# Optimization experiments

Hardware: AMD Instinct MI355X
Metric: run time of the kernel (lower is better)

Reference implementation:

```python
import jax, jax.numpy as jnp
import numpy as np

B, S, H, NH, DH, I, C, P = 4, 1024, 1280, 20, 64, 5120, 13, 8
LN_EPS = 1e-5


def setup_inputs() -> dict:
    key = jax.random.key(0)
    ks = jax.random.split(key, 20)
    n = lambda k, shp, s=0.02: (jax.random.normal(k, shp, jnp.float32) * s)
    return {
        "hidden_states": jax.random.normal(ks[0], (B, S, H), jnp.float32),
        "attention_mask": jnp.ones((B, S), jnp.float32),
        "Wq": n(ks[1], (H, H)), "bq": jnp.zeros((H,), jnp.float32),
        "Wk": n(ks[2], (H, H)), "bk": jnp.zeros((H,), jnp.float32),
        "Wv": n(ks[3], (H, H)), "bv": jnp.zeros((H,), jnp.float32),
        "W_ct1": n(ks[4], (P, C), 0.3), "b_ct1": jnp.zeros((P,), jnp.float32),
        "W_ct2": n(ks[5], (P, C), 0.3), "b_ct2": jnp.zeros((P,), jnp.float32),
        "M": n(ks[6], (C, C), 0.5),
        "bias_scale": jnp.full((1,), 0.5, jnp.float32),
        "W_ptm": n(ks[7], (P, H)), "b_ptm": jnp.zeros((P,), jnp.float32),
        "ln_g": jnp.ones((H,), jnp.float32), "ln_b": jnp.zeros((H,), jnp.float32),
        "Wf1": n(ks[8], (I, H)), "bf1": jnp.zeros((I,), jnp.float32),
        "Wf2": n(ks[9], (H, I)), "bf2": jnp.zeros((H,), jnp.float32),
    }


def reference(hidden_states, attention_mask, Wq, bq, Wk, bk, Wv, bv,
              W_ct1, b_ct1, W_ct2, b_ct2, M, bias_scale, W_ptm, b_ptm,
              ln_g, ln_b, Wf1, bf1, Wf2, bf2):
    h = hidden_states
    # crosstalk bilinear projection: (P,C) @ (C,P) -> (P,P)
    out1 = (M.T @ W_ct1.T + b_ct1).T          # (P, C)
    out2 = M @ W_ct2.T + b_ct2                # (C, P)
    R = out1 @ out2                           # (P, P)
    # ptm_predictor (Linear H->P) + softmax
    ptm = jax.nn.softmax(h @ W_ptm.T + b_ptm, axis=-1)            # (B,S,P)
    Bb = jnp.tanh(jnp.einsum('blc,cd,bmd->blm', ptm, R, ptm)) * bias_scale  # (B,S,S)
    # manual multi-head attention
    q = (h @ Wq.T + bq).reshape(B, S, NH, DH).transpose(0, 2, 1, 3)
    k = (h @ Wk.T + bk).reshape(B, S, NH, DH).transpose(0, 2, 1, 3)
    v = (h @ Wv.T + bv).reshape(B, S, NH, DH).transpose(0, 2, 1, 3)
    scores = jnp.einsum('bhld,bhmd->bhlm', q, k) / np.float32(np.sqrt(DH))
    scores = scores + Bb[:, None]
    scores = scores + (1.0 - attention_mask)[:, None, None, :] * jnp.finfo(h.dtype).min
    probs = jax.nn.softmax(scores, axis=-1)
    ctx = jnp.einsum('bhlm,bhmd->bhld', probs, v)
    ctx = ctx.transpose(0, 2, 1, 3).reshape(B, S, H)
    # residual + LayerNorm
    x = h + ctx
    mu = jnp.mean(x, -1, keepdims=True)
    var = jnp.var(x, -1, keepdims=True)
    x = (x - mu) * jax.lax.rsqrt(var + LN_EPS) * ln_g + ln_b
    # FFN with exact GELU, residual
    ff = jax.nn.gelu(x @ Wf1.T + bf1, approximate=False) @ Wf2.T + bf2
    return x + ff
```

## Files before the change

### kernel.cpp

```cpp
#include <hip/hip_runtime.h>
#include <math.h>

typedef _Float16 f16;
typedef _Float16 f16x2 __attribute__((ext_vector_type(2)));
typedef _Float16 f16x8 __attribute__((ext_vector_type(8)));
typedef _Float16 f16x4 __attribute__((ext_vector_type(4)));
typedef float f32x4 __attribute__((ext_vector_type(4)));

#define B_ 4
#define S_ 1024
#define H_ 1280
#define NH_ 20
#define DH_ 64
#define I_ 5120
#define C_ 13
#define P_ 8
#define QS_ 3840
#define LOG2E 1.44269504088896f

__device__ __forceinline__ void store_val(float* p, float v) { *p = v; }
__device__ __forceinline__ void store_val(f16* p, float v) { *p = (f16)v; }

__device__ __forceinline__ float fast_gelu(float x) {
    float ax = 0.70710678118654752f * fabsf(x);
    float t = __builtin_amdgcn_rcpf(1.0f + 0.3275911f * ax);
    float p = t * (0.254829592f + t * (-0.284496736f + t * (1.421413741f
              + t * (-1.453152027f + t * 1.061405429f))));
    float e = __builtin_exp2f(-(LOG2E) * ax * ax);
    float er = 1.0f - p * e;
    float cdf = 0.5f + 0.5f * (x >= 0.0f ? er : -er);
    return x * cdf;
}

__device__ __forceinline__ float fast_tanh(float x) {
    x = fminf(fmaxf(x, -20.0f), 20.0f);
    float e = __builtin_exp2f(x * (2.0f * LOG2E));
    return (e - 1.0f) * __builtin_amdgcn_rcpf(e + 1.0f);
}

__global__ __launch_bounds__(256) void prep_kernel(const float* __restrict__ hin,
                                                   const float* __restrict__ Wptm,
                                                   const float* __restrict__ bptm,
                                                   const float* __restrict__ Mg,
                                                   const float* __restrict__ W1,
                                                   const float* __restrict__ b1,
                                                   const float* __restrict__ W2,
                                                   const float* __restrict__ b2,
                                                   float* __restrict__ ptm,
                                                   float* __restrict__ tg,
                                                   f16* __restrict__ hin16,
                                                   const float* __restrict__ Wq,
                                                   const float* __restrict__ Wk,
                                                   const float* __restrict__ Wv,
                                                   const float* __restrict__ Wf1,
                                                   const float* __restrict__ Wf2,
                                                   f16* __restrict__ Wq16,
                                                   f16* __restrict__ Wk16,
                                                   f16* __restrict__ Wv16,
                                                   f16* __restrict__ Wf116,
                                                   f16* __restrict__ Wf216) {
    const int bid = blockIdx.x;
    int t = threadIdx.x;
    if (bid >= 1024) {
        const int cb = bid - 1024;
        const float* src; f16* dst; int base;
        if (cb < 4800) {
            const int s = cb / 1600;
            src = (s == 0) ? Wq : (s == 1) ? Wk : Wv;
            dst = (s == 0) ? Wq16 : (s == 1) ? Wk16 : Wv16;
            base = (cb - s * 1600) * 256;
        } else if (cb < 11200) {
            src = Wf1; dst = Wf116; base = (cb - 4800) * 256;
        } else {
            src = Wf2; dst = Wf216; base = (cb - 11200) * 256;
        }
        const int i = base + t;
        f32x4 v = ((const f32x4*)src)[i];
        f16x4 o;
#pragma unroll
        for (int e = 0; e < 4; e++) o[e] = (f16)v[e];
        ((f16x4*)dst)[i] = o;
        return;
    }

    __shared__ float o1[P_][C_];
    __shared__ float o2[C_][P_];
    __shared__ float R[P_ * P_];
    if (t < P_ * C_) {
        int p = t / C_, c = t % C_;
        float s = b1[p];
        for (int k = 0; k < C_; k++) s += Mg[k * C_ + c] * W1[p * C_ + k];
        o1[p][c] = s;
        int c2 = t / P_, p2 = t % P_;
        float s2 = b2[p2];
        for (int k = 0; k < C_; k++) s2 += Mg[c2 * C_ + k] * W2[p2 * C_ + k];
        o2[c2][p2] = s2;
    }
    __syncthreads();
    if (t < P_ * P_) {
        int p = t >> 3, q = t & 7;
        float s = 0.f;
        for (int c = 0; c < C_; c++) s += o1[p][c] * o2[c][q];
        R[t] = s;
    }
    __syncthreads();

    int wv = t >> 6, lane = t & 63;
    int row = bid * 4 + wv;
    const float* hrow = hin + (size_t)row * H_;
    f16* hrow16 = hin16 + (size_t)row * H_;
    float acc[P_] = {};
    for (int i = 0; i < H_ / 64; i++) {
        int k = lane + 64 * i;
        float hv = hrow[k];
        hrow16[k] = (f16)hv;
#pragma unroll
        for (int p = 0; p < P_; p++) acc[p] += hv * Wptm[p * H_ + k];
    }
#pragma unroll
    for (int p = 0; p < P_; p++) {
#pragma unroll
        for (int o = 32; o >= 1; o >>= 1) acc[p] += __shfl_xor(acc[p], o);
        acc[p] += bptm[p];
    }
    float mx = acc[0];
#pragma unroll
    for (int p = 1; p < P_; p++) mx = fmaxf(mx, acc[p]);
    float sum = 0.f;
#pragma unroll
    for (int p = 0; p < P_; p++) { acc[p] = expf(acc[p] - mx); sum += acc[p]; }
    float rinv = 1.f / sum;
#pragma unroll
    for (int p = 0; p < P_; p++) acc[p] *= rinv;
    float tv[P_];
#pragma unroll
    for (int d = 0; d < P_; d++) {
        float s = 0.f;
#pragma unroll
        for (int c = 0; c < P_; c++) s += acc[c] * R[c * P_ + d];
        tv[d] = s;
    }
    if (lane == 0) {
#pragma unroll
        for (int p = 0; p < P_; p++) {
            ptm[(size_t)row * P_ + p] = acc[p];
            tg[(size_t)row * P_ + p]  = tv[p];
        }
    }
}

__global__ __launch_bounds__(256) void bias_kernel(const float* __restrict__ tg,
                                                   const float* __restrict__ ptm,
                                                   const float* __restrict__ mask,
                                                   const float* __restrict__ bscale_p,
                                                   f16* __restrict__ bb) {
    const int bl = blockIdx.x;
    const int b = bl >> 10;
    const int t = threadIdx.x;
    __shared__ float tl[P_];
    if (t < P_) tl[t] = tg[(size_t)bl * P_ + t];
    __syncthreads();
    const float bscale = bscale_p[0];
    float t0 = tl[0], t1 = tl[1], t2 = tl[2], t3 = tl[3];
    float t4 = tl[4], t5 = tl[5], t6 = tl[6], t7 = tl[7];
#pragma unroll
    for (int i = 0; i < 4; i++) {
        int m = t + 256 * i;
        const float* pm = ptm + ((size_t)b * S_ + m) * P_;
        float4 p0 = *(const float4*)pm;
        float4 p1 = *(const float4*)(pm + 4);
        float d = t0 * p0.x + t1 * p0.y + t2 * p0.z + t3 * p0.w
                + t4 * p1.x + t5 * p1.y + t6 * p1.z + t7 * p1.w;
        float v = (fast_tanh(d) * bscale + (1.0f - mask[(size_t)b * S_ + m]) * (-30000.0f)) * LOG2E;
        bb[(size_t)bl * S_ + m] = (f16)v;
    }
}

template <int MODE, typename YT>
__device__ __forceinline__ void gemm_body(const f16* __restrict__ X,
                                          const f16* __restrict__ W,
                                          const float* __restrict__ bias,
                                          YT* __restrict__ Y,
                                          int Ndim, int Kdim, int kbeg, int kend,
                                          int m0, int n0, f16* sA, f16* sB) {
    const int t = threadIdx.x;
    const int lane = t & 63, w = t >> 6;
    const int wr = w >> 1, wc = w & 1;
    const int lr = lane & 15, kq = lane >> 4;

    f32x4 acc[4][4] = {};

    int s_row[4], s_gc[4];
#pragma unroll
    for (int inst = 0; inst < 4; inst++) {
        int ci = t + 256 * inst;
        s_row[inst] = ci >> 3;
        s_gc[inst] = (ci & 7) ^ (s_row[inst] & 7);
    }

    for (int k0 = kbeg; k0 < kend; k0 += 64) {
        __syncthreads();
#pragma unroll
        for (int inst = 0; inst < 4; inst++) {
            int ci = t + 256 * inst;
            __builtin_amdgcn_global_load_lds(
                (const unsigned*)(X + (size_t)(m0 + s_row[inst]) * Kdim + k0 + s_gc[inst] * 8),
                (unsigned*)(sA + ci * 8), 16, 0, 0);
        }
#pragma unroll
        for (int inst = 0; inst < 4; inst++) {
            int ci = t + 256 * inst;
            __builtin_amdgcn_global_load_lds(
                (const unsigned*)(W + (size_t)(n0 + s_row[inst]) * Kdim + k0 + s_gc[inst] * 8),
                (unsigned*)(sB + ci * 8), 16, 0, 0);
        }
        __syncthreads();
#pragma unroll
        for (int ks = 0; ks < 2; ks++) {
            f16x8 af[4], bf[4];
#pragma unroll
            for (int i = 0; i < 4; i++) {
                int row = wr * 64 + i * 16 + lr;
                int cl = (ks * 4 + kq) ^ (row & 7);
                af[i] = *(const f16x8*)(sA + row * 64 + cl * 8);
            }
#pragma unroll
            for (int j = 0; j < 4; j++) {
                int row = wc * 64 + j * 16 + lr;
                int cl = (ks * 4 + kq) ^ (row & 7);
                bf[j] = *(const f16x8*)(sB + row * 64 + cl * 8);
            }
#pragma unroll
            for (int i = 0; i < 4; i++)
#pragma unroll
                for (int j = 0; j < 4; j++)
                    acc[i][j] = __builtin_amdgcn_mfma_f32_16x16x32_f16(af[i], bf[j], acc[i][j], 0, 0, 0);
        }
    }
#pragma unroll
    for (int j = 0; j < 4; j++) {
        int col = n0 + wc * 64 + j * 16 + lr;
        float bcol = bias[col];
#pragma unroll
        for (int i = 0; i < 4; i++) {
#pragma unroll
            for (int rr = 0; rr < 4; rr++) {
                int row = m0 + wr * 64 + i * 16 + kq * 4 + rr;
                float v = acc[i][j][rr] + bcol;
                if (MODE == 1) v = fast_gelu(v);
                store_val(&Y[(size_t)row * Ndim + col], v);
            }
        }
    }
}

template <int MODE, typename YT>
__global__ __launch_bounds__(256, 2) void gemm128(const f16* __restrict__ X,
                                                  const f16* __restrict__ W,
                                                  const float* __restrict__ bias,
                                                  YT* __restrict__ Y,
                                                  int Ndim, int Kdim) {
    __shared__ f16 sA[128 * 64];
    __shared__ f16 sB[128 * 64];
    gemm_body<MODE, YT>(X, W, bias, Y, Ndim, Kdim, 0, Kdim,
                        blockIdx.x * 128, blockIdx.y * 128, sA, sB);
}

template <int MODE, typename YT>
__device__ __forceinline__ void g256_body(const f16* __restrict__ X,
                                          const f16* __restrict__ W,
                                          const float* __restrict__ bias,
                                          YT* __restrict__ Y,
                                          int Ndim, int Kdim, int kbeg, int kend,
                                          int m0, int n0, f16* sA, f16* sB) {
    const int NT = (kend - kbeg) >> 6;
    const int t = threadIdx.x;
    const int lane = t & 63, w = t >> 6;
    const int wr = w >> 2, wc = w & 3;
    const int lr = lane & 15, kq = lane >> 4;

    const int rh0 = t >> 3;
    const int gc0 = (t & 7) ^ (rh0 & 7);
    const f16* Asrc = X + (size_t)(m0 + rh0) * Kdim + kbeg + gc0 * 8;
    const f16* Bsrc = W + (size_t)(n0 + rh0) * Kdim + kbeg + gc0 * 8;

    f32x4 acc[8][4] = {};

#define STG_A(kt_) do { f16* d_ = sA + ((kt_) & 1) * 16384 + t * 8;            \
        const f16* s_ = Asrc + (size_t)(kt_) * 64;                             \
        __builtin_amdgcn_global_load_lds((const unsigned*)s_, (unsigned*)d_, 16, 0, 0); \
        __builtin_amdgcn_global_load_lds((const unsigned*)(s_ + (size_t)64 * Kdim),  (unsigned*)(d_ + 4096), 16, 0, 0);  \
        __builtin_amdgcn_global_load_lds((const unsigned*)(s_ + (size_t)128 * Kdim), (unsigned*)(d_ + 8192), 16, 0, 0);  \
        __builtin_amdgcn_global_load_lds((const unsigned*)(s_ + (size_t)192 * Kdim), (unsigned*)(d_ + 12288), 16, 0, 0); \
    } while (0)
#define STG_B(kt_) do { f16* d_ = sB + ((kt_) & 1) * 16384 + t * 8;            \
        const f16* s_ = Bsrc + (size_t)(kt_) * 64;                             \
        __builtin_amdgcn_global_load_lds((const unsigned*)s_, (unsigned*)d_, 16, 0, 0); \
        __builtin_amdgcn_global_load_lds((const unsigned*)(s_ + (size_t)64 * Kdim),  (unsigned*)(d_ + 4096), 16, 0, 0);  \
        __builtin_amdgcn_global_load_lds((const unsigned*)(s_ + (size_t)128 * Kdim), (unsigned*)(d_ + 8192), 16, 0, 0);  \
        __builtin_amdgcn_global_load_lds((const unsigned*)(s_ + (size_t)192 * Kdim), (unsigned*)(d_ + 12288), 16, 0, 0); \
    } while (0)

    STG_A(0); STG_B(0);
    if (NT > 1) {
        STG_A(1); STG_B(1);
        asm volatile("s_waitcnt vmcnt(8)");
    } else {
        asm volatile("s_waitcnt vmcnt(0)");
    }
    __builtin_amdgcn_s_barrier();

    for (int kt = 0; kt < NT; ++kt) {
        const int p = kt & 1;
        const f16* cA = sA + p * 16384;
        const f16* cB = sB + p * 16384;
        f16x8 a[4][2], b0[2][2], b1[2][2];

#pragma unroll
        for (int i = 0; i < 4; ++i) {
            const int r = wr * 128 + (i + 4) * 16 + lr;
#pragma unroll
            for (int ks = 0; ks < 2; ++ks)
                a[i][ks] = *(const f16x8*)(cA + r * 64 + (((ks * 4 + kq) ^ (r & 7)) * 8));
        }
#pragma unroll
        for (int j = 0; j < 2; ++j) {
            const int rb = wc * 64 + j * 16 + lr;
#pragma unroll
            for (int ks = 0; ks < 2; ++ks)
                b0[j][ks] = *(const f16x8*)(cB + rb * 64 + (((ks * 4 + kq) ^ (rb & 7)) * 8));
        }
        __builtin_amdgcn_s_barrier();
        __builtin_amdgcn_s_setprio(1);
#pragma unroll
        for (int ks = 0; ks < 2; ++ks)
#pragma unroll
            for (int i = 0; i < 4; ++i)
#pragma unroll
                for (int j = 0; j < 2; ++j)
                    acc[i + 4][j] = __builtin_amdgcn_mfma_f32_16x16x32_f16(
                        a[i][ks], b0[j][ks], acc[i + 4][j], 0, 0, 0);
        __builtin_amdgcn_s_setprio(0);
        __builtin_amdgcn_s_barrier();

#pragma unroll
        for (int j = 0; j < 2; ++j) {
            const int rb = wc * 64 + (j + 2) * 16 + lr;
#pragma unroll
            for (int ks = 0; ks < 2; ++ks)
                b1[j][ks] = *(const f16x8*)(cB + rb * 64 + (((ks * 4 + kq) ^ (rb & 7)) * 8));
        }
        __builtin_amdgcn_s_barrier();
        __builtin_amdgcn_s_setprio(1);
#pragma unroll
        for (int ks = 0; ks < 2; ++ks)
#pragma unroll
            for (int i = 0; i < 4; ++i)
#pragma unroll
                for (int j = 0; j < 2; ++j)
                    acc[i + 4][j + 2] = __builtin_amdgcn_mfma_f32_16x16x32_f16(
                        a[i][ks], b1[j][ks], acc[i + 4][j + 2], 0, 0, 0);
        __builtin_amdgcn_s_setprio(0);
        __builtin_amdgcn_s_barrier();

#pragma unroll
        for (int i = 0; i < 4; ++i) {
            const int r = wr * 128 + i * 16 + lr;
#pragma unroll
            for (int ks = 0; ks < 2; ++ks)
                a[i][ks] = *(const f16x8*)(cA + r * 64 + (((ks * 4 + kq) ^ (r & 7)) * 8));
        }
        if (kt + 2 < NT) STG_B(kt + 2);
        __builtin_amdgcn_s_barrier();
        __builtin_amdgcn_s_setprio(1);
#pragma unroll
        for (int ks = 0; ks < 2; ++ks)
#pragma unroll
            for (int i = 0; i < 4; ++i)
#pragma unroll
                for (int j = 0; j < 2; ++j)
                    acc[i][j] = __builtin_amdgcn_mfma_f32_16x16x32_f16(
                        a[i][ks], b0[j][ks], acc[i][j], 0, 0, 0);
        __builtin_amdgcn_s_setprio(0);
        __builtin_amdgcn_s_barrier();

        if (kt + 2 < NT) STG_A(kt + 2);
        __builtin_amdgcn_s_setprio(1);
#pragma unroll
        for (int ks = 0; ks < 2; ++ks)
#pragma unroll
            for (int i = 0; i < 4; ++i)
#pragma unroll
                for (int j = 0; j < 2; ++j)
                    acc[i][j + 2] = __builtin_amdgcn_mfma_f32_16x16x32_f16(
                        a[i][ks], b1[j][ks], acc[i][j + 2], 0, 0, 0);
        __builtin_amdgcn_s_setprio(0);
        if (kt + 2 < NT) asm volatile("s_waitcnt vmcnt(8)");
        else             asm volatile("s_waitcnt vmcnt(0)");
        __builtin_amdgcn_s_barrier();
    }
#undef STG_A
#undef STG_B

#pragma unroll
    for (int j = 0; j < 4; ++j) {
        const int col = n0 + wc * 64 + j * 16 + lr;
        const float bcol = (MODE == 3) ? 0.f : bias[col];
#pragma unroll
        for (int i = 0; i < 8; ++i) {
#pragma unroll
            for (int rr = 0; rr < 4; ++rr) {
                const int row = m0 + wr * 128 + i * 16 + kq * 4 + rr;
                float v = acc[i][j][rr] + bcol;
                store_val(&Y[(size_t)row * Ndim + col], v);
            }
        }
    }
}

__global__ __launch_bounds__(512, 2) void gemm256_sk(const f16* __restrict__ X,
                                                     const f16* __restrict__ W,
                                                     float* __restrict__ p0,
                                                     float* __restrict__ p1,
                                                     float* __restrict__ p2,
                                                     int Ndim, int Kdim) {
    __shared__ f16 sA[2 * 16384];
    __shared__ f16 sB[2 * 16384];
    const int z = blockIdx.z;
    float* __restrict__ Y = (z == 0) ? p0 : (z == 1) ? p1 : p2;
    const int kbeg = z * 1728;
    const int kend = (z == 2) ? Kdim : kbeg + 1728;
    g256_body<3, float>(X, W, nullptr, Y, Ndim, Kdim, kbeg, kend,
                        blockIdx.x * 256, blockIdx.y * 256, sA, sB);
}

__global__ __launch_bounds__(512, 2) void gemm256_qkv(const f16* __restrict__ X,
                                                      const f16* __restrict__ Wqkv,
                                                      const float* __restrict__ bq,
                                                      const float* __restrict__ bk,
                                                      const float* __restrict__ bv,
                                                      f16* __restrict__ Y) {
    __shared__ f16 sA[2 * 16384];
    __shared__ f16 sB[2 * 16384];
    const int nt = blockIdx.y;
    const int g = nt / 5;
    const float* bsel = (g == 0) ? bq : (g == 1) ? bk : bv;
    g256_body<0, f16>(X, Wqkv, bsel - (size_t)g * 1280, Y, QS_, H_, 0, H_,
                      blockIdx.x * 256, nt * 256, sA, sB);
}

__global__ __launch_bounds__(256) void reduce3_kernel(const float* __restrict__ p0,
                                                      const float* __restrict__ p1,
                                                      const float* __restrict__ p2,
                                                      const float* __restrict__ bias,
                                                      const f16* __restrict__ res,
                                                      float* __restrict__ out) {
    int i = blockIdx.x * 256 + threadIdx.x;
    int col = (i * 4) % H_;
    f32x4 a = ((const f32x4*)p0)[i];
    f32x4 b = ((const f32x4*)p1)[i];
    f32x4 c = ((const f32x4*)p2)[i];
    f32x4 bc = *(const f32x4*)(bias + col);
    f16x4 r = ((const f16x4*)res)[i];
    f32x4 o;
#pragma unroll
    for (int e = 0; e < 4; e++) o[e] = a[e] + b[e] + c[e] + bc[e] + (float)r[e];
    ((f32x4*)out)[i] = o;
}

__global__ __launch_bounds__(256) void attn_kernel(const f16* __restrict__ qkv,
                                                   const f16* __restrict__ bb,
                                                   const float* __restrict__ hin,
                                                   float* __restrict__ xpre) {
    __shared__ f16 sK[64 * 72];
    __shared__ f16 sVT[64 * 72];
    __shared__ f16 sP[64 * 72];

    const int t = threadIdx.x;
    const int w = t >> 6, lane = t & 63;
    const int lr = lane & 15, kq = lane >> 4;
    const int gid = blockIdx.x + 16 * (blockIdx.y + 20 * blockIdx.z);
    const int wk = (gid & 7) * 160 + (gid >> 3);
    const int l0 = (wk & 15) * 64;
    const int hb = wk >> 4;
    const int h = hb % 20, b = hb / 20;
    const size_t base  = (size_t)b * S_ * H_ + (size_t)h * DH_;
    const size_t baseq = (size_t)b * S_ * QS_ + (size_t)h * DH_;
    const size_t kbase = baseq + 1280;
    const size_t vbase = baseq + 2560;

    const int kr0 = t >> 3, kc8 = (t & 7) * 8;
    const int vr2 = (t >> 3) * 2, vc8 = (t & 7) * 8;
    const int vmsw = vr2 ^ vc8;
    const int br = t >> 2, bc16 = (t & 3) * 16;
    const f16* bbrow0 = bb + ((size_t)b * S_ + l0 + br) * S_;

    f16x8 kA0 = *(const f16x8*)&qkv[kbase + (size_t)kr0 * QS_ + kc8];
    f16x8 kA1 = *(const f16x8*)&qkv[kbase + (size_t)(kr0 + 32) * QS_ + kc8];
    f16x8 vA0 = *(const f16x8*)&qkv[vbase + (size_t)vr2 * QS_ + vc8];
    f16x8 vA1 = *(const f16x8*)&qkv[vbase + (size_t)(vr2 + 1) * QS_ + vc8];
    f16x8 bA0 = *(const f16x8*)(bbrow0 + bc16);
    f16x8 bA1 = *(const f16x8*)(bbrow0 + bc16 + 8);

    f16x8 afq[2];
#pragma unroll
    for (int ks = 0; ks < 2; ks++) {
        f16x8 qv = *(const f16x8*)&qkv[baseq + (size_t)(l0 + w * 16 + lr) * QS_ + ks * 32 + kq * 8];
#pragma unroll
        for (int e = 0; e < 8; e++) qv[e] = (f16)((float)qv[e] * (0.125f * LOG2E));
        afq[ks] = qv;
    }

    f32x4 acc_o[4] = {};
    float lstate[4] = {};

    for (int mt = 0; mt < 16; mt++) {
        __syncthreads();
        *(f16x8*)&sK[kr0 * 72 + kc8] = kA0;
        *(f16x8*)&sK[(kr0 + 32) * 72 + kc8] = kA1;
#pragma unroll
        for (int e = 0; e < 8; e++) {
            f16x2 pk = {vA0[e], vA1[e]};
            *(f16x2*)&sVT[(vc8 + e) * 72 + vmsw] = pk;
        }
        *(f16x8*)&sP[br * 72 + bc16] = bA0;
        *(f16x8*)&sP[br * 72 + bc16 + 8] = bA1;
        const int m1 = ((mt + 1) & 15) * 64;
        f16x8 kB0 = *(const f16x8*)&qkv[kbase + (size_t)(m1 + kr0) * QS_ + kc8];
        f16x8 kB1 = *(const f16x8*)&qkv[kbase + (size_t)(m1 + kr0 + 32) * QS_ + kc8];
        f16x8 vB0 = *(const f16x8*)&qkv[vbase + (size_t)(m1 + vr2) * QS_ + vc8];
        f16x8 vB1 = *(const f16x8*)&qkv[vbase + (size_t)(m1 + vr2 + 1) * QS_ + vc8];
        f16x8 bB0 = *(const f16x8*)(bbrow0 + m1 + bc16);
        f16x8 bB1 = *(const f16x8*)(bbrow0 + m1 + bc16 + 8);
        __syncthreads();

        f32x4 sacc[4] = {};
        __builtin_amdgcn_s_setprio(1);
#pragma unroll
        for (int ks = 0; ks < 2; ks++)
#pragma unroll
            for (int j = 0; j < 4; j++) {
                f16x8 bk = *(const f16x8*)&sK[(j * 16 + lr) * 72 + ks * 32 + kq * 8];
                sacc[j] = __builtin_amdgcn_mfma_f32_16x16x32_f16(afq[ks], bk, sacc[j], 0, 0, 0);
            }
        __builtin_amdgcn_s_setprio(0);

#pragma unroll
        for (int j = 0; j < 4; j++)
#pragma unroll
            for (int rr = 0; rr < 4; rr++) {
                const int sp_addr = (w * 16 + kq * 4 + rr) * 72 + j * 16 + lr;
                float p = __builtin_exp2f(sacc[j][rr] + (float)sP[sp_addr]);
                lstate[rr] += p;
                sP[sp_addr] = (f16)p;
            }

        f16x8 ap[2];
        ap[0] = *(const f16x8*)&sP[(w * 16 + lr) * 72 + kq * 8];
        ap[1] = *(const f16x8*)&sP[(w * 16 + lr) * 72 + 32 + kq * 8];
        __builtin_amdgcn_s_setprio(1);
#pragma unroll
        for (int ks = 0; ks < 2; ks++)
#pragma unroll
            for (int j2 = 0; j2 < 4; j2++) {
                int d = j2 * 16 + lr;
                int s_ = (d >> 3) & 7;
                f16x8 bv = *(const f16x8*)&sVT[d * 72 + 8 * (((ks << 2) + kq) ^ s_)];
                acc_o[j2] = __builtin_amdgcn_mfma_f32_16x16x32_f16(ap[ks], bv, acc_o[j2], 0, 0, 0);
            }
        __builtin_amdgcn_s_setprio(0);
        kA0 = kB0; kA1 = kB1; vA0 = vB0; vA1 = vB1; bA0 = bB0; bA1 = bB1;
    }

#pragma unroll
    for (int rr = 0; rr < 4; rr++) {
#pragma unroll
        for (int off = 8; off >= 1; off >>= 1) lstate[rr] += __shfl_xor(lstate[rr], off);
    }

#pragma unroll
    for (int rr = 0; rr < 4; rr++) {
        float linv = 1.0f / lstate[rr];
        int tok = l0 + w * 16 + kq * 4 + rr;
        size_t obase = base + (size_t)tok * H_;
#pragma unroll
        for (int j2 = 0; j2 < 4; j2++) {
            int d = j2 * 16 + lr;
            xpre[obase + d] = hin[obase + d] + acc_o[j2][rr] * linv;
        }
    }
}

__global__ __launch_bounds__(256) void ln_kernel(const float* __restrict__ xpre,
                                                 const float* __restrict__ g,
                                                 const float* __restrict__ bb,
                                                 f16* __restrict__ xln) {
    int row = blockIdx.x, t = threadIdx.x;
    const float* xr = xpre + (size_t)row * H_;
    float xv[5], s1 = 0.f, s2 = 0.f;
#pragma unroll
    for (int i = 0; i < 5; i++) {
        float v = xr[t + 256 * i];
        xv[i] = v; s1 += v; s2 += v * v;
    }
#pragma unroll
    for (int o = 32; o >= 1; o >>= 1) { s1 += __shfl_xor(s1, o); s2 += __shfl_xor(s2, o); }
    __shared__ float r1[4], r2[4];
    int wv = t >> 6, lane = t & 63;
    if (lane == 0) { r1[wv] = s1; r2[wv] = s2; }
    __syncthreads();
    float m1 = (r1[0] + r1[1] + r1[2] + r1[3]) * (1.0f / H_);
    float m2 = (r2[0] + r2[1] + r2[2] + r2[3]) * (1.0f / H_);
    float rstd = rsqrtf(m2 - m1 * m1 + 1e-5f);
#pragma unroll
    for (int i = 0; i < 5; i++) {
        int c = t + 256 * i;
        float v = (xv[i] - m1) * rstd * g[c] + bb[c];
        xln[(size_t)row * H_ + c] = (f16)v;
    }
}

extern "C" void kernel_launch(void* const* d_in, const int* in_sizes, int n_in,
                              void* d_out, int out_size, void* d_ws, size_t ws_size,
                              hipStream_t stream) {
    (void)in_sizes; (void)n_in; (void)out_size; (void)ws_size;
    const float* hin  = (const float*)d_in[0];
    const float* mask = (const float*)d_in[1];
    const float* Wq = (const float*)d_in[2];  const float* bq = (const float*)d_in[3];
    const float* Wk = (const float*)d_in[4];  const float* bk = (const float*)d_in[5];
    const float* Wv = (const float*)d_in[6];  const float* bv = (const float*)d_in[7];
    const float* Wct1 = (const float*)d_in[8];  const float* bct1 = (const float*)d_in[9];
    const float* Wct2 = (const float*)d_in[10]; const float* bct2 = (const float*)d_in[11];
    const float* Mg = (const float*)d_in[12];   const float* bscale = (const float*)d_in[13];
    const float* Wptm = (const float*)d_in[14]; const float* bptm = (const float*)d_in[15];
    const float* lng = (const float*)d_in[16];  const float* lnb = (const float*)d_in[17];
    const float* Wf1 = (const float*)d_in[18];  const float* bf1 = (const float*)d_in[19];
    const float* Wf2 = (const float*)d_in[20];  const float* bf2 = (const float*)d_in[21];

    char* ws = (char*)d_ws;
    const size_t SZ_PT  = (size_t)B_ * S_ * P_ * 4;
    const size_t SZ_H16 = (size_t)B_ * S_ * H_ * 2;
    const size_t SZ_H32 = (size_t)B_ * S_ * H_ * 4;
    const size_t SZ_WH  = (size_t)H_ * H_ * 2;
    const size_t SZ_WI  = (size_t)I_ * H_ * 2;
    float* ptm  = (float*)(ws + 256);
    float* tg   = (float*)(ws + 256 + SZ_PT);
    char* A0    = ws + 256 + 2 * SZ_PT;
    f16* hin16  = (f16*)(A0);
    f16* qkvb   = (f16*)(A0 + SZ_H16);
    float* xpre = (float*)(A0 + 4 * SZ_H16);
    f16* xln    = (f16*)(A0 + 4 * SZ_H16 + SZ_H32);
    f16* bbias  = (f16*)(A0 + 5 * SZ_H16 + SZ_H32);
    char* WA    = A0 + 5 * SZ_H16 + SZ_H32 + (size_t)B_ * S_ * S_ * 2;
    f16* Wq16   = (f16*)(WA);
    f16* Wk16   = (f16*)(WA + SZ_WH);
    f16* Wv16   = (f16*)(WA + 2 * SZ_WH);
    f16* Wf116  = (f16*)(WA + 3 * SZ_WH);
    f16* Wf216  = (f16*)(WA + 3 * SZ_WH + SZ_WI);
    f16* g1     = (f16*)(A0);
    float* pbuf = (float*)(WA + 3 * SZ_WH + 2 * SZ_WI);

    prep_kernel<<<1024 + 17600, 256, 0, stream>>>(
        hin, Wptm, bptm, Mg, Wct1, bct1, Wct2, bct2, ptm, tg, hin16,
        Wq, Wk, Wv, Wf1, Wf2, Wq16, Wk16, Wv16, Wf116, Wf216);
    bias_kernel<<<B_ * S_, 256, 0, stream>>>(tg, ptm, mask, bscale, bbias);
    gemm256_qkv<<<dim3(16, 15), 512, 0, stream>>>(hin16, Wq16, bq, bk, bv, qkvb);
    attn_kernel<<<dim3(S_ / 64, NH_, B_), 256, 0, stream>>>(qkvb, bbias, hin, xpre);
    ln_kernel<<<B_ * S_, 256, 0, stream>>>(xpre, lng, lnb, xln);
    gemm128<1, f16><<<dim3(32, I_ / 128), 256, 0, stream>>>(xln, Wf116, bf1, g1, I_, H_);
    gemm256_sk<<<dim3(16, H_ / 256, 3), 512, 0, stream>>>(
        g1, Wf216, pbuf, pbuf + (size_t)B_ * S_ * H_, xpre, H_, I_);
    reduce3_kernel<<<(B_ * S_ * H_) / 4 / 256, 256, 0, stream>>>(
        pbuf, pbuf + (size_t)B_ * S_ * H_, xpre, bf2, xln, (float*)d_out);
}
```

Baseline: 422.2 us.

## Process 128 query rows per attention block to reuse K/V tiles

Each attention workgroup now covers 128 query rows instead of 64. Every wave handles two 16-row query groups against the same K and V shared-memory tiles, so the grid is halved and each K/V tile load and transpose is amortized over twice as many queries. The cost is more registers for the doubled accumulators and score tiles, a larger shared P/bias buffer, and half as many blocks, which could reduce occupancy and leave part of the GPU idle.

```diff
diff --git a/kernel.cpp b/kernel.cpp
--- a/kernel.cpp
+++ b/kernel.cpp
@@ -474,15 +474,15 @@
                                                    float* __restrict__ xpre) {
     __shared__ f16 sK[64 * 72];
     __shared__ f16 sVT[64 * 72];
-    __shared__ f16 sP[64 * 72];
+    __shared__ f16 sP[128 * 72];
 
     const int t = threadIdx.x;
     const int w = t >> 6, lane = t & 63;
     const int lr = lane & 15, kq = lane >> 4;
-    const int gid = blockIdx.x + 16 * (blockIdx.y + 20 * blockIdx.z);
-    const int wk = (gid & 7) * 160 + (gid >> 3);
-    const int l0 = (wk & 15) * 64;
-    const int hb = wk >> 4;
+    const int gid = blockIdx.x + 8 * (blockIdx.y + 20 * blockIdx.z);
+    const int wk = (gid & 7) * 80 + (gid >> 3);
+    const int l0 = (wk & 7) * 128;
+    const int hb = wk >> 3;
     const int h = hb % 20, b = hb / 20;
     const size_t base  = (size_t)b * S_ * H_ + (size_t)h * DH_;
     const size_t baseq = (size_t)b * S_ * QS_ + (size_t)h * DH_;
@@ -494,6 +494,7 @@
     const int vmsw = vr2 ^ vc8;
     const int br = t >> 2, bc16 = (t & 3) * 16;
     const f16* bbrow0 = bb + ((size_t)b * S_ + l0 + br) * S_;
+    const f16* bbrow1 = bbrow0 + (size_t)64 * S_;
 
     f16x8 kA0 = *(const f16x8*)&qkv[kbase + (size_t)kr0 * QS_ + kc8];
     f16x8 kA1 = *(const f16x8*)&qkv[kbase + (size_t)(kr0 + 32) * QS_ + kc8];
@@ -501,18 +502,23 @@
     f16x8 vA1 = *(const f16x8*)&qkv[vbase + (size_t)(vr2 + 1) * QS_ + vc8];
     f16x8 bA0 = *(const f16x8*)(bbrow0 + bc16);
     f16x8 bA1 = *(const f16x8*)(bbrow0 + bc16 + 8);
-
-    f16x8 afq[2];
-#pragma unroll
-    for (int ks = 0; ks < 2; ks++) {
-        f16x8 qv = *(const f16x8*)&qkv[baseq + (size_t)(l0 + w * 16 + lr) * QS_ + ks * 32 + kq * 8];
-#pragma unroll
-        for (int e = 0; e < 8; e++) qv[e] = (f16)((float)qv[e] * (0.125f * LOG2E));
-        afq[ks] = qv;
-    }
-
-    f32x4 acc_o[4] = {};
-    float lstate[4] = {};
+    f16x8 bA2 = *(const f16x8*)(bbrow1 + bc16);
+    f16x8 bA3 = *(const f16x8*)(bbrow1 + bc16 + 8);
+
+    f16x8 afq[2][2];
+#pragma unroll
+    for (int g = 0; g < 2; g++)
+#pragma unroll
+        for (int ks = 0; ks < 2; ks++) {
+            f16x8 qv = *(const f16x8*)&qkv[baseq +
+                (size_t)(l0 + g * 64 + w * 16 + lr) * QS_ + ks * 32 + kq * 8];
+#pragma unroll
+            for (int e = 0; e < 8; e++) qv[e] = (f16)((float)qv[e] * (0.125f * LOG2E));
+            afq[g][ks] = qv;
+        }
+
+    f32x4 acc_o[2][4] = {};
+    float lstate[2][4] = {};
 
     for (int mt = 0; mt < 16; mt++) {
         __syncthreads();
@@ -525,6 +531,8 @@
         }
         *(f16x8*)&sP[br * 72 + bc16] = bA0;
         *(f16x8*)&sP[br * 72 + bc16 + 8] = bA1;
+        *(f16x8*)&sP[(br + 64) * 72 + bc16] = bA2;
+        *(f16x8*)&sP[(br + 64) * 72 + bc16 + 8] = bA3;
         const int m1 = ((mt + 1) & 15) * 64;
         f16x8 kB0 = *(const f16x8*)&qkv[kbase + (size_t)(m1 + kr0) * QS_ + kc8];
         f16x8 kB1 = *(const f16x8*)&qkv[kbase + (size_t)(m1 + kr0 + 32) * QS_ + kc8];
@@ -532,63 +540,80 @@
         f16x8 vB1 = *(const f16x8*)&qkv[vbase + (size_t)(m1 + vr2 + 1) * QS_ + vc8];
         f16x8 bB0 = *(const f16x8*)(bbrow0 + m1 + bc16);
         f16x8 bB1 = *(const f16x8*)(bbrow0 + m1 + bc16 + 8);
+        f16x8 bB2 = *(const f16x8*)(bbrow1 + m1 + bc16);
+        f16x8 bB3 = *(const f16x8*)(bbrow1 + m1 + bc16 + 8);
         __syncthreads();
 
-        f32x4 sacc[4] = {};
+        f32x4 sacc[2][4] = {};
         __builtin_amdgcn_s_setprio(1);
 #pragma unroll
-        for (int ks = 0; ks < 2; ks++)
-#pragma unroll
-            for (int j = 0; j < 4; j++) {
-                f16x8 bk = *(const f16x8*)&sK[(j * 16 + lr) * 72 + ks * 32 + kq * 8];
-                sacc[j] = __builtin_amdgcn_mfma_f32_16x16x32_f16(afq[ks], bk, sacc[j], 0, 0, 0);
-            }
+        for (int g = 0; g < 2; g++)
+#pragma unroll
+            for (int ks = 0; ks < 2; ks++)
+#pragma unroll
+                for (int j = 0; j < 4; j++) {
+                    f16x8 bk = *(const f16x8*)&sK[(j * 16 + lr) * 72 + ks * 32 + kq * 8];
+                    sacc[g][j] = __builtin_amdgcn_mfma_f32_16x16x32_f16(
+                        afq[g][ks], bk, sacc[g][j], 0, 0, 0);
+                }
         __builtin_amdgcn_s_setprio(0);
 
 #pragma unroll
-        for (int j = 0; j < 4; j++)
-#pragma unroll
-            for (int rr = 0; rr < 4; rr++) {
-                const int sp_addr = (w * 16 + kq * 4 + rr) * 72 + j * 16 + lr;
-                float p = __builtin_exp2f(sacc[j][rr] + (float)sP[sp_addr]);
-                lstate[rr] += p;
-                sP[sp_addr] = (f16)p;
-            }
-
-        f16x8 ap[2];
-        ap[0] = *(const f16x8*)&sP[(w * 16 + lr) * 72 + kq * 8];
-        ap[1] = *(const f16x8*)&sP[(w * 16 + lr) * 72 + 32 + kq * 8];
+        for (int g = 0; g < 2; g++)
+#pragma unroll
+            for (int j = 0; j < 4; j++)
+#pragma unroll
+                for (int rr = 0; rr < 4; rr++) {
+                    const int sp_addr = (g * 64 + w * 16 + kq * 4 + rr) * 72 + j * 16 + lr;
+                    float p = __builtin_exp2f(sacc[g][j][rr] + (float)sP[sp_addr]);
+                    lstate[g][rr] += p;
+                    sP[sp_addr] = (f16)p;
+                }
+
         __builtin_amdgcn_s_setprio(1);
 #pragma unroll
-        for (int ks = 0; ks < 2; ks++)
+        for (int g = 0; g < 2; g++) {
+            f16x8 ap[2];
+            ap[0] = *(const f16x8*)&sP[(g * 64 + w * 16 + lr) * 72 + kq * 8];
+            ap[1] = *(const f16x8*)&sP[(g * 64 + w * 16 + lr) * 72 + 32 + kq * 8];
+#pragma unroll
+            for (int ks = 0; ks < 2; ks++)
+#pragma unroll
+                for (int j2 = 0; j2 < 4; j2++) {
+                    int d = j2 * 16 + lr;
+                    int s_ = (d >> 3) & 7;
+                    f16x8 bv = *(const f16x8*)&sVT[d * 72 + 8 * (((ks << 2) + kq) ^ s_)];
+                    acc_o[g][j2] = __builtin_amdgcn_mfma_f32_16x16x32_f16(
+                        ap[ks], bv, acc_o[g][j2], 0, 0, 0);
+                }
+        }
+        __builtin_amdgcn_s_setprio(0);
+        kA0 = kB0; kA1 = kB1; vA0 = vB0; vA1 = vB1;
+        bA0 = bB0; bA1 = bB1; bA2 = bB2; bA3 = bB3;
+    }
+
+#pragma unroll
+    for (int g = 0; g < 2; g++)
+#pragma unroll
+        for (int rr = 0; rr < 4; rr++) {
+#pragma unroll
+            for (int off = 8; off >= 1; off >>= 1)
+                lstate[g][rr] += __shfl_xor(lstate[g][rr], off);
+        }
+
+#pragma unroll
+    for (int g = 0; g < 2; g++)
+#pragma unroll
+        for (int rr = 0; rr < 4; rr++) {
+            float linv = 1.0f / lstate[g][rr];
+            int tok = l0 + g * 64 + w * 16 + kq * 4 + rr;
+            size_t obase = base + (size_t)tok * H_;
 #pragma unroll
             for (int j2 = 0; j2 < 4; j2++) {
                 int d = j2 * 16 + lr;
-                int s_ = (d >> 3) & 7;
-                f16x8 bv = *(const f16x8*)&sVT[d * 72 + 8 * (((ks << 2) + kq) ^ s_)];
-                acc_o[j2] = __builtin_amdgcn_mfma_f32_16x16x32_f16(ap[ks], bv, acc_o[j2], 0, 0, 0);
+                xpre[obase + d] = hin[obase + d] + acc_o[g][j2][rr] * linv;
             }
-        __builtin_amdgcn_s_setprio(0);
-        kA0 = kB0; kA1 = kB1; vA0 = vB0; vA1 = vB1; bA0 = bB0; bA1 = bB1;
-    }
-
-#pragma unroll
-    for (int rr = 0; rr < 4; rr++) {
-#pragma unroll
-        for (int off = 8; off >= 1; off >>= 1) lstate[rr] += __shfl_xor(lstate[rr], off);
-    }
-
-#pragma unroll
-    for (int rr = 0; rr < 4; rr++) {
-        float linv = 1.0f / lstate[rr];
-        int tok = l0 + w * 16 + kq * 4 + rr;
-        size_t obase = base + (size_t)tok * H_;
-#pragma unroll
-        for (int j2 = 0; j2 < 4; j2++) {
-            int d = j2 * 16 + lr;
-            xpre[obase + d] = hin[obase + d] + acc_o[j2][rr] * linv;
-        }
-    }
+        }
 }
 
 __global__ __launch_bounds__(256) void ln_kernel(const float* __restrict__ xpre,
@@ -665,7 +690,7 @@
         Wq, Wk, Wv, Wf1, Wf2, Wq16, Wk16, Wv16, Wf116, Wf216);
     bias_kernel<<<B_ * S_, 256, 0, stream>>>(tg, ptm, mask, bscale, bbias);
     gemm256_qkv<<<dim3(16, 15), 512, 0, stream>>>(hin16, Wq16, bq, bk, bv, qkvb);
-    attn_kernel<<<dim3(S_ / 64, NH_, B_), 256, 0, stream>>>(qkvb, bbias, hin, xpre);
+    attn_kernel<<<dim3(S_ / 128, NH_, B_), 256, 0, stream>>>(qkvb, bbias, hin, xpre);
     ln_kernel<<<B_ * S_, 256, 0, stream>>>(xpre, lng, lnb, xln);
     gemm128<1, f16><<<dim3(32, I_ / 128), 256, 0, stream>>>(xln, Wf116, bf1, g1, I_, H_);
     gemm256_sk<<<dim3(16, H_ / 256, 3), 512, 0, stream>>>(
```

Result: slower. 454.8 us (+7.7%).
